# Kernel tuning notes

Hardware: AMD Instinct MI355X
Metric: run time of the kernel (lower is better)

## Reference

```python
import jax, jax.numpy as jnp
import numpy as np

D_STATE = 16
D_CONV = 4

def layernorm(x, g, b, eps=1e-5):
    m = jnp.mean(x, -1, keepdims=True)
    v = jnp.var(x, -1, keepdims=True)
    return (x - m) / jnp.sqrt(v + eps) * g + b

def conv1x1(x, w):  # x [b,h,w,cin], w [cin,cout]
    return jnp.einsum('bhwc,cd->bhwd', x, w)

def dwconv3x3(x, w):  # x [b,h,w,C], w [3,3,1,C] (HWIO, groups=C)
    return jax.lax.conv_general_dilated(x, w, (1, 1), 'SAME',
        dimension_numbers=('NHWC', 'HWIO', 'NHWC'),
        feature_group_count=x.shape[-1])

def causal_dwconv1d(x, w, b):  # x [B,L,D], w [K,1,D]; causal depthwise conv (Mamba d_conv=4)
    xp = jnp.pad(x, ((0, 0), (D_CONV - 1, 0), (0, 0)))
    y = jax.lax.conv_general_dilated(xp, w, (1,), 'VALID',
        dimension_numbers=('NWC', 'WIO', 'NWC'),
        feature_group_count=x.shape[-1])
    return y + b

def selective_scan(deltaA, deltaBx, C):
    # deltaA, deltaBx: [B,L,D,S]; C: [B,L,S] -> y: [B,L,D]
    def step(h, inp):
        dA, dBx, c = inp
        h = dA * h + dBx
        return h, jnp.einsum('bds,bs->bd', h, c)
    h0 = jnp.zeros(deltaA.shape[:1] + deltaA.shape[2:], deltaA.dtype)
    _, ys = jax.lax.scan(step, h0,
        (jnp.swapaxes(deltaA, 0, 1), jnp.swapaxes(deltaBx, 0, 1), jnp.swapaxes(C, 0, 1)))
    return jnp.swapaxes(ys, 0, 1)

def spa_ssm(x, in_w, conv_w, conv_b, xproj_w, dt_w, dt_b, Alog, D, out_w):
    # Mamba (slow path) applied to flattened spatial sequence; x: [b,h,w,c]
    b, h, w, c = x.shape
    L = h * w
    xs = x.reshape(b, L, c)
    di = Alog.shape[0]
    xz = xs @ in_w                       # [b,L,2*di]
    xi, z = xz[..., :di], xz[..., di:]
    xi = jax.nn.silu(causal_dwconv1d(xi, conv_w, conv_b))
    dbc = xi @ xproj_w                   # [b,L,dt_rank+2*S]
    dtr = dt_w.shape[0]
    dt = jax.nn.softplus(dbc[..., :dtr] @ dt_w + dt_b)   # [b,L,di]
    B = dbc[..., dtr:dtr + D_STATE]
    C = dbc[..., dtr + D_STATE:]
    A = -jnp.exp(Alog)                   # [di,S]
    deltaA = jnp.exp(dt[..., None] * A)                  # [b,L,di,S]
    deltaBx = (dt * xi)[..., None] * B[:, :, None, :]    # [b,L,di,S]
    y = selective_scan(deltaA, deltaBx, C) + D * xi
    y = y * jax.nn.silu(z)
    return (y @ out_w).reshape(b, h, w, c)

def camba_forward(x, ln1_g, ln1_b, vin_w1, vin_dw, vin_w2, vout_dw1, vout_dw2,
                  ssm_in_w, ssm_conv_w, ssm_conv_b, ssm_xproj_w, ssm_dt_w, ssm_dt_b,
                  ssm_Alog, ssm_D, ssm_out_w, ln2_g, ln2_b, ff_w1, ff_dw, ff_w2):
    x = jnp.transpose(x, (0, 2, 3, 1))   # [b,h,w,c]
    # ESSM: v_in_head = LN -> 1x1 -> dw3x3 -> GELU -> 1x1
    x0 = conv1x1(layernorm(x, ln1_g, ln1_b), vin_w1)
    x0 = jax.nn.gelu(dwconv3x3(x0, vin_dw), approximate=False)
    x0 = conv1x1(x0, vin_w2)
    y = spa_ssm(x0, ssm_in_w, ssm_conv_w, ssm_conv_b, ssm_xproj_w,
                ssm_dt_w, ssm_dt_b, ssm_Alog, ssm_D, ssm_out_w) + x0
    # v_out_head = dw3x3 -> GELU -> dw3x3, residual
    y = dwconv3x3(jax.nn.gelu(dwconv3x3(y, vout_dw1), approximate=False), vout_dw2) + y
    x = y + x                            # block residual
    # PreNorm FeedForward (mult=4): 1x1 -> LReLU -> dw3x3 -> LReLU -> 1x1
    t = layernorm(x, ln2_g, ln2_b)
    t = jax.nn.leaky_relu(conv1x1(t, ff_w1), 0.2)
    t = jax.nn.leaky_relu(dwconv3x3(t, ff_dw), 0.2)
    t = conv1x1(t, ff_w2)
    x = t + x
    return jnp.transpose(x, (0, 3, 1, 2))

def setup_inputs() -> dict:
    key = jax.random.key(0)
    ks = jax.random.split(key, 16)
    b, c, h, w = 8, 64, 64, 64
    di, ds, dtr = 128, 16, 4
    s = 0.05
    n = lambda k, shp: jax.random.normal(k, shp, jnp.float32) * s
    dt0 = jnp.exp(jax.random.uniform(ks[1], (di,)) * (np.log(0.1) - np.log(1e-3)) + np.log(1e-3))
    return dict(
        x=jax.random.normal(ks[0], (b, c, h, w), jnp.float32),
        ln1_g=jnp.ones(c), ln1_b=jnp.zeros(c),
        vin_w1=n(ks[2], (c, c)), vin_dw=n(ks[3], (3, 3, 1, c)), vin_w2=n(ks[4], (c, c)),
        vout_dw1=n(ks[5], (3, 3, 1, c)), vout_dw2=n(ks[6], (3, 3, 1, c)),
        ssm_in_w=n(ks[7], (c, 2 * di)),
        ssm_conv_w=n(ks[8], (D_CONV, 1, di)), ssm_conv_b=jnp.zeros(di),
        ssm_xproj_w=n(ks[9], (di, dtr + 2 * ds)),
        ssm_dt_w=n(ks[10], (dtr, di)), ssm_dt_b=jnp.log(jnp.expm1(dt0)),
        ssm_Alog=jnp.log(jnp.broadcast_to(jnp.arange(1., ds + 1), (di, ds))),
        ssm_D=jnp.ones(di),
        ssm_out_w=n(ks[11], (di, c)),
        ln2_g=jnp.ones(c), ln2_b=jnp.zeros(c),
        ff_w1=n(ks[12], (c, 4 * c)), ff_dw=n(ks[13], (3, 3, 1, 4 * c)), ff_w2=n(ks[14], (4 * c, c)),
    )

def reference(x, ln1_g, ln1_b, vin_w1, vin_dw, vin_w2, vout_dw1, vout_dw2,
              ssm_in_w, ssm_conv_w, ssm_conv_b, ssm_xproj_w, ssm_dt_w, ssm_dt_b,
              ssm_Alog, ssm_D, ssm_out_w, ln2_g, ln2_b, ff_w1, ff_dw, ff_w2):
    return camba_forward(x, ln1_g, ln1_b, vin_w1, vin_dw, vin_w2, vout_dw1, vout_dw2,
                         ssm_in_w, ssm_conv_w, ssm_conv_b, ssm_xproj_w, ssm_dt_w, ssm_dt_b,
                         ssm_Alog, ssm_D, ssm_out_w, ln2_g, ln2_b, ff_w1, ff_dw, ff_w2)
```

## Files before the change

kernel.cpp:

```cpp
#include <hip/hip_runtime.h>
#include <hip/hip_bf16.h>
#include <math.h>

typedef unsigned short u16;
typedef __attribute__((ext_vector_type(8))) short s8v;
typedef __attribute__((ext_vector_type(4))) float f4v;

#define B_    8
#define C_    64
#define HW_   4096
#define NPIX  32768
#define DI    128
#define NCH   256
#define CHL   16

__device__ __forceinline__ float b2f(u16 v){ return __uint_as_float(((unsigned)v)<<16); }
__device__ __forceinline__ u16 f2b(float x){
  unsigned u = __float_as_uint(x);
  u += 0x7fff + ((u >> 16) & 1);
  return (u16)(u >> 16);
}
__device__ __forceinline__ float gelu_exact(float x){ return 0.5f*x*(1.0f+erff(x*0.70710678118654752f)); }
__device__ __forceinline__ float leaky02(float x){ return x>0.f ? x : 0.2f*x; }
__device__ __forceinline__ float softplus_(float x){ return fmaxf(x,0.f)+log1pf(__expf(-fabsf(x))); }
__device__ __forceinline__ float silu_(float x){ return x / (1.0f + __expf(-x)); }
__device__ __forceinline__ void unpack16(uint4 q0, uint4 q1, float* v){
  unsigned w[8]={q0.x,q0.y,q0.z,q0.w,q1.x,q1.y,q1.z,q1.w};
  #pragma unroll
  for(int j=0;j<8;j++){
    v[2*j]   = __uint_as_float(w[j]<<16);
    v[2*j+1] = __uint_as_float(w[j]&0xffff0000u);
  }
}

__global__ void k_prep(const float* __restrict__ vin_w1, const float* __restrict__ vin_w2,
                       const float* __restrict__ ssm_in_w, const float* __restrict__ xproj,
                       const float* __restrict__ dtw, const float* __restrict__ ssm_outw,
                       const float* __restrict__ ff_w1, const float* __restrict__ ff_w2,
                       u16* __restrict__ wv1, u16* __restrict__ wv2, u16* __restrict__ wsi,
                       u16* __restrict__ wdb, u16* __restrict__ wout, u16* __restrict__ wf1,
                       u16* __restrict__ wf2t){
  int g = blockIdx.x*256 + threadIdx.x;
  if(g < 4096){
    int n=g>>6, c=g&63;
    wv1[n*64+c]=f2b(vin_w1[c*64+n]);
    wv2[n*64+c]=f2b(vin_w2[c*64+n]);
  }
  if(g < 16384){
    int n=g>>6, c=g&63;
    wsi[n*64+c]=f2b(ssm_in_w[c*256+n]);
    wf1[n*64+c]=f2b(ff_w1[c*256+n]);
    int n2=g/256, k2=g%256;
    wf2t[n2*256+k2]=f2b(ff_w2[k2*64+n2]);
  }
  if(g < 8192){
    int n=g>>7, k=g&127;
    wout[n*128+k]=f2b(ssm_outw[k*64+n]);
  }
  if(g < 20480){
    int n=g/128, k=g%128;
    float v;
    if(n < 128){
      v = 0.f;
      for(int r=0;r<4;r++) v += xproj[k*36+r]*dtw[r*128+n];
    }else{
      v = xproj[k*36+4+(n-128)];
    }
    wdb[n*128+k]=f2b(v);
  }
}

__global__ __launch_bounds__(256) void k_trans_ln_mm(const float* __restrict__ x,
                     const float* __restrict__ g, const float* __restrict__ bta,
                     const u16* __restrict__ wT,
                     u16* __restrict__ xT, u16* __restrict__ outp){
  const int LDA = 72, NS = 4;
  __shared__ float tile[64][65];
  __shared__ __align__(16) u16 sA[64*LDA];
  __shared__ __align__(16) u16 sW[64*LDA];
  int tid = threadIdx.x;
  int blk = blockIdx.x;
  int b = blk >> 6;
  int hwb = (blk & 63) << 6;
  int lane = tid & 63, row = tid >> 6;
  const float* src = x + (size_t)b*C_*HW_;
  #pragma unroll
  for(int k=0;k<16;k++){
    int c = row + 4*k;
    tile[c][lane] = src[c*HW_ + hwb + lane];
  }
  for(int idx=tid; idx<64*8; idx+=256){
    int n = idx>>3, c8 = (idx&7)*8;
    *(uint4*)(sW + n*LDA + c8) = *(const uint4*)(wT + n*64 + c8);
  }
  __syncthreads();
  u16* dstT = xT + (size_t)b*HW_*C_;
  #pragma unroll
  for(int k=0;k<16;k++){
    int hwl = row + 4*k;
    dstT[(hwb+hwl)*C_ + lane] = f2b(tile[lane][hwl]);
  }
  float gg = g[lane], bb = bta[lane];
  #pragma unroll
  for(int i=0;i<16;i++){
    int hwl = row*16 + i;
    float v = tile[lane][hwl];
    float s = v, sq = v*v;
    #pragma unroll
    for(int o=32;o>0;o>>=1){ s += __shfl_xor(s,o); sq += __shfl_xor(sq,o); }
    float m = s*(1.f/64.f);
    float var = sq*(1.f/64.f) - m*m;
    float r = rsqrtf(var + 1e-5f);
    sA[hwl*LDA + lane] = f2b((v-m)*r*gg + bb);
  }
  __syncthreads();
  int ln = tid & 63, wv = tid >> 6;
  int mrow = ln & 15, quad = ln >> 4;
  f4v acc[NS];
  #pragma unroll
  for(int i=0;i<NS;i++) acc[i] = (f4v){0.f,0.f,0.f,0.f};
  const u16* aBase = sA + (wv*16 + mrow)*LDA + quad*8;
  const u16* wBase = sW + mrow*LDA + quad*8;
  #pragma unroll
  for(int kk=0; kk<64; kk+=32){
    s8v af = *(const s8v*)(aBase + kk);
    #pragma unroll
    for(int ns=0; ns<NS; ns++){
      s8v bf = *(const s8v*)(wBase + ns*16*LDA + kk);
      acc[ns] = __builtin_amdgcn_mfma_f32_16x16x32_bf16(af, bf, acc[ns], 0, 0, 0);
    }
  }
  int p0 = blk*64;
  int pr = p0 + wv*16 + quad*4;
  #pragma unroll
  for(int ns=0; ns<NS; ns++){
    int n = ns*16 + mrow;
    #pragma unroll
    for(int r=0;r<4;r++)
      outp[(size_t)(pr+r)*64 + n] = f2b(acc[ns][r]);
  }
}

__global__ __launch_bounds__(256) void k_dw3mm(const u16* __restrict__ in,
                     const float* __restrict__ dwgt, const u16* __restrict__ wT,
                     u16* __restrict__ x0){
  const int LDT = 72;
  __shared__ __align__(16) u16 sIn[10*10*64];
  __shared__ __align__(16) u16 sT[64*LDT];
  __shared__ __align__(16) u16 sW[64*LDT];
  int tid = threadIdx.x;
  int blk = blockIdx.x;
  int b = blk >> 6;
  int t6 = blk & 63;
  int h0 = (t6 >> 3) * 8, w0 = (t6 & 7) * 8;
  for(int idx=tid; idx<64*8; idx+=256){
    int n = idx>>3, c8 = (idx&7)*8;
    *(uint4*)(sW + n*LDT + c8) = *(const uint4*)(wT + n*64 + c8);
  }
  for(int q=tid; q<10*10*16; q+=256){
    int pp = q >> 4, c4 = q & 15;
    int hh = pp / 10, ww = pp % 10;
    int gh = h0-1+hh, gw = w0-1+ww;
    ushort4 v = make_ushort4(0,0,0,0);
    if((unsigned)gh < 64u && (unsigned)gw < 64u)
      v = *(const ushort4*)(in + (size_t)((b*64+gh)*64+gw)*64 + c4*4);
    *(ushort4*)(sIn + pp*64 + c4*4) = v;
  }
  __syncthreads();
  int c4 = tid & 15;
  #pragma unroll
  for(int pass=0; pass<4; pass++){
    int opix = pass*16 + (tid>>4);
    int oh = opix >> 3, ow = opix & 7;
    float a0=0.f,a1=0.f,a2=0.f,a3=0.f;
    #pragma unroll
    for(int kh=0;kh<3;kh++){
      #pragma unroll
      for(int kw=0;kw<3;kw++){
        ushort4 v = *(const ushort4*)(sIn + ((oh+kh)*10 + (ow+kw))*64 + c4*4);
        float4 wv = *(const float4*)(dwgt + (kh*3+kw)*64 + c4*4);
        a0 += b2f(v.x)*wv.x; a1 += b2f(v.y)*wv.y;
        a2 += b2f(v.z)*wv.z; a3 += b2f(v.w)*wv.w;
      }
    }
    ushort4 o; o.x=f2b(gelu_exact(a0)); o.y=f2b(gelu_exact(a1));
    o.z=f2b(gelu_exact(a2)); o.w=f2b(gelu_exact(a3));
    *(ushort4*)(sT + opix*LDT + c4*4) = o;
  }
  __syncthreads();
  int ln = tid & 63, wv = tid >> 6;
  int mrow = ln & 15, quad = ln >> 4;
  f4v acc[4];
  #pragma unroll
  for(int i=0;i<4;i++) acc[i] = (f4v){0.f,0.f,0.f,0.f};
  const u16* aBase = sT + (wv*16 + mrow)*LDT + quad*8;
  const u16* wBase = sW + mrow*LDT + quad*8;
  #pragma unroll
  for(int kk=0; kk<64; kk+=32){
    s8v af = *(const s8v*)(aBase + kk);
    #pragma unroll
    for(int ns=0; ns<4; ns++){
      s8v bf = *(const s8v*)(wBase + ns*16*LDT + kk);
      acc[ns] = __builtin_amdgcn_mfma_f32_16x16x32_bf16(af, bf, acc[ns], 0, 0, 0);
    }
  }
  #pragma unroll
  for(int ns=0; ns<4; ns++){
    int n = ns*16 + mrow;
    #pragma unroll
    for(int r=0;r<4;r++){
      int opix = wv*16 + quad*4 + r;
      int oh = opix >> 3, ow = opix & 7;
      size_t p = ((size_t)(b*64 + h0+oh)*64 + (w0+ow));
      x0[p*64 + n] = f2b(acc[ns][r]);
    }
  }
}

template<int CIN, int COUT, int ACT, bool OUTF32>
__global__ __launch_bounds__(256) void k_mfma(const u16* __restrict__ wT,
                     const u16* __restrict__ in, const float* __restrict__ bias,
                     const u16* __restrict__ res, void* __restrict__ outv){
  const int KCH = (CIN < 128) ? CIN : 128;
  const int LDA = KCH + 8;
  const int NS  = COUT / 16;
  __shared__ __align__(16) u16 sA[64*LDA];
  __shared__ __align__(16) u16 sW[COUT*LDA];
  int tid = threadIdx.x;
  int p0 = blockIdx.x * 64;
  int ln = tid & 63, wv = tid >> 6;
  int mrow = ln & 15, quad = ln >> 4;
  f4v acc[NS];
  #pragma unroll
  for(int i=0;i<NS;i++) acc[i] = (f4v){0.f,0.f,0.f,0.f};
  const u16* aBase = sA + (wv*16 + mrow)*LDA + quad*8;
  const u16* wBase = sW + mrow*LDA + quad*8;
  const int RW = KCH/8;
  for(int k0=0; k0<CIN; k0+=KCH){
    if(k0) __syncthreads();
    for(int idx=tid; idx<COUT*RW; idx+=256){
      int n = idx/RW, c8 = (idx%RW)*8;
      *(uint4*)(sW + n*LDA + c8) = *(const uint4*)(wT + (size_t)n*CIN + k0 + c8);
    }
    for(int g=tid; g<64*RW; g+=256){
      int row = g / RW, c8 = (g % RW)*8;
      *(uint4*)(sA + row*LDA + c8) = *(const uint4*)(in + (size_t)(p0+row)*CIN + k0 + c8);
    }
    __syncthreads();
    #pragma unroll
    for(int kk=0; kk<KCH; kk+=32){
      s8v af = *(const s8v*)(aBase + kk);
      #pragma unroll
      for(int ns=0; ns<NS; ns++){
        s8v bf = *(const s8v*)(wBase + ns*16*LDA + kk);
        acc[ns] = __builtin_amdgcn_mfma_f32_16x16x32_bf16(af, bf, acc[ns], 0, 0, 0);
      }
    }
  }
  int pr = p0 + wv*16 + quad*4;
  #pragma unroll
  for(int ns=0; ns<NS; ns++){
    int n = ns*16 + mrow;
    float bs = bias ? bias[n] : 0.f;
    #pragma unroll
    for(int r=0;r<4;r++){
      float v = acc[ns][r] + bs;
      if(ACT==1) v = leaky02(v);
      else if(ACT==2) v = softplus_(v);
      if(res) v += b2f(res[(size_t)(pr+r)*COUT + n]);
      if(OUTF32) ((float*)outv)[(size_t)(pr+r)*COUT + n] = v;
      else       ((u16*)outv)[(size_t)(pr+r)*COUT + n] = f2b(v);
    }
  }
}

__global__ __launch_bounds__(256) void k_ssm_dtbc(const u16* __restrict__ wT,
                     const u16* __restrict__ x0,
                     const float* __restrict__ cw, const float* __restrict__ cb,
                     const u16* __restrict__ wdb, const float* __restrict__ dtbias,
                     u16* __restrict__ xi, u16* __restrict__ zs,
                     u16* __restrict__ dtout, u16* __restrict__ bcout){
  const int LDA=72, NS=16, LDY=136, LDWD=136, NS2=10;
  __shared__ __align__(16) u16 S[31616];
  u16* sW   = S;
  u16* sA   = S + 18432;
  u16* ubuf = S + 23040;
  u16* xiT  = S;
  u16* wdbS = S + 8704;
  int tid = threadIdx.x;
  int p0 = blockIdx.x*64;
  int ln = tid & 63, wv = tid >> 6;
  int mrow = ln & 15, quad = ln >> 4;
  for(int idx=tid; idx<256*8; idx+=256){
    int n = idx>>3, c8 = (idx&7)*8;
    *(uint4*)(sW + n*LDA + c8) = *(const uint4*)(wT + n*64 + c8);
  }
  for(int g=tid; g<64*8; g+=256){
    int row = g >> 3, c8 = (g & 7)*8;
    *(uint4*)(sA + row*LDA + c8) = *(const uint4*)(x0 + (size_t)(p0+row)*64 + c8);
  }
  __syncthreads();
  f4v acc[NS];
  #pragma unroll
  for(int i=0;i<NS;i++) acc[i] = (f4v){0.f,0.f,0.f,0.f};
  const u16* aBase = sA + (wv*16 + mrow)*LDA + quad*8;
  const u16* wBase = sW + mrow*LDA + quad*8;
  #pragma unroll
  for(int kk=0; kk<64; kk+=32){
    s8v af = *(const s8v*)(aBase + kk);
    #pragma unroll
    for(int ns=0; ns<NS; ns++){
      s8v bf = *(const s8v*)(wBase + ns*16*LDA + kk);
      acc[ns] = __builtin_amdgcn_mfma_f32_16x16x32_bf16(af, bf, acc[ns], 0, 0, 0);
    }
  }
  bool bstart = ((p0 & 4095) == 0);
  for(int idx=tid; idx<384; idx+=256){
    int j = idx >> 7, n = idx & 127;
    float a2 = 0.f;
    if(!bstart){
      const u16* xr = x0 + (size_t)(p0-3+j)*64;
      #pragma unroll 8
      for(int c=0;c<64;c++) a2 += b2f(xr[c]) * b2f(sW[n*LDA+c]);
    }
    ubuf[j*128 + n] = f2b(a2);
  }
  int prl = wv*16 + quad*4;
  #pragma unroll
  for(int ns=0; ns<NS; ns++){
    int n = ns*16 + mrow;
    if(n < 128){
      #pragma unroll
      for(int r=0;r<4;r++) ubuf[(prl+r+3)*128 + n] = f2b(acc[ns][r]);
    }else{
      #pragma unroll
      for(int r=0;r<4;r++) zs[(size_t)(p0+prl+r)*128 + (n-128)] = f2b(silu_(acc[ns][r]));
    }
  }
  __syncthreads();
  int d4 = tid & 31;
  float4 cbv = *(const float4*)(cb + d4*4);
  for(int row = tid >> 5; row < 64; row += 8){
    float a0=cbv.x, a1=cbv.y, a2=cbv.z, a3=cbv.w;
    #pragma unroll
    for(int k=0;k<4;k++){
      ushort4 v = *(const ushort4*)(ubuf + (row+k)*128 + d4*4);
      float4 wv4 = *(const float4*)(cw + k*128 + d4*4);
      a0 += b2f(v.x)*wv4.x; a1 += b2f(v.y)*wv4.y;
      a2 += b2f(v.z)*wv4.z; a3 += b2f(v.w)*wv4.w;
    }
    ushort4 o; o.x=f2b(silu_(a0)); o.y=f2b(silu_(a1)); o.z=f2b(silu_(a2)); o.w=f2b(silu_(a3));
    *(ushort4*)(xi + (size_t)(p0+row)*128 + d4*4) = o;
    *(ushort4*)(xiT + row*LDY + d4*4) = o;
  }
  __syncthreads();
  for(int idx=tid; idx<160*16; idx+=256){
    int n = idx>>4, c8 = (idx&15)*8;
    *(uint4*)(wdbS + n*LDWD + c8) = *(const uint4*)(wdb + n*128 + c8);
  }
  __syncthreads();
  f4v acc2[NS2];
  #pragma unroll
  for(int i=0;i<NS2;i++) acc2[i] = (f4v){0.f,0.f,0.f,0.f};
  #pragma unroll
  for(int kk=0; kk<128; kk+=32){
    s8v af = *(const s8v*)(xiT + (wv*16+mrow)*LDY + kk + quad*8);
    #pragma unroll
    for(int ns=0; ns<NS2; ns++){
      s8v bf = *(const s8v*)(wdbS + (ns*16+mrow)*LDWD + kk + quad*8);
      acc2[ns] = __builtin_amdgcn_mfma_f32_16x16x32_bf16(af, bf, acc2[ns], 0, 0, 0);
    }
  }
  int pr = p0 + wv*16 + quad*4;
  #pragma unroll
  for(int ns=0; ns<NS2; ns++){
    int n = ns*16 + mrow;
    if(n < 128){
      float bs = dtbias[n];
      #pragma unroll
      for(int r=0;r<4;r++)
        dtout[(size_t)(pr+r)*128 + n] = f2b(softplus_(acc2[ns][r] + bs));
    }else{
      #pragma unroll
      for(int r=0;r<4;r++)
        bcout[(size_t)(pr+r)*32 + (n-128)] = f2b(acc2[ns][r]);
    }
  }
}

__global__ __launch_bounds__(256) void k_scan1(const u16* __restrict__ dt, const u16* __restrict__ xi,
                        const u16* __restrict__ bc, const float* __restrict__ alog,
                        u16* __restrict__ Pb, u16* __restrict__ Qb){
  int t = blockIdx.x*256 + threadIdx.x;
  int d = t & 127;
  int ch = (t >> 7) & 255;
  int b = t >> 15;
  int pbase = b*HW_ + ch*CHL;
  float A[16];
  #pragma unroll
  for(int s=0;s<16;s++) A[s] = -__expf(alog[d*16+s]);
  float dtv[16], uv[16];
  #pragma unroll
  for(int i=0;i<CHL;i++){
    dtv[i] = b2f(dt[(size_t)(pbase+i)*128 + d]);
    uv[i]  = dtv[i] * b2f(xi[(size_t)(pbase+i)*128 + d]);
  }
  float Q[16], sumdt = 0.f;
  #pragma unroll
  for(int s=0;s<16;s++) Q[s] = 0.f;
  #pragma unroll
  for(int i=0;i<CHL;i++){
    float Bv[16];
    unpack16(*(const uint4*)(bc + (size_t)(pbase+i)*32),
             *(const uint4*)(bc + (size_t)(pbase+i)*32 + 8), Bv);
    sumdt += dtv[i];
    #pragma unroll
    for(int s=0;s<16;s++){
      float a = __expf(dtv[i]*A[s]);
      Q[s] = a*Q[s] + uv[i]*Bv[s];
    }
  }
  int gidx = ch*16384 + (b*128+d)*16;
  unsigned pw[8], qw[8];
  #pragma unroll
  for(int j=0;j<8;j++){
    pw[j] = (unsigned)f2b(__expf(A[2*j]*sumdt)) | ((unsigned)f2b(__expf(A[2*j+1]*sumdt))<<16);
    qw[j] = (unsigned)f2b(Q[2*j]) | ((unsigned)f2b(Q[2*j+1])<<16);
  }
  *(uint4*)(Pb+gidx)   = make_uint4(pw[0],pw[1],pw[2],pw[3]);
  *(uint4*)(Pb+gidx+8) = make_uint4(pw[4],pw[5],pw[6],pw[7]);
  *(uint4*)(Qb+gidx)   = make_uint4(qw[0],qw[1],qw[2],qw[3]);
  *(uint4*)(Qb+gidx+8) = make_uint4(qw[4],qw[5],qw[6],qw[7]);
}

__global__ void k_scan2(const u16* __restrict__ Pb, const u16* __restrict__ Qb,
                        u16* __restrict__ Hin){
  int g2 = (blockIdx.x*64 + threadIdx.x)*2;
  float h0 = 0.f, h1 = 0.f;
  #pragma unroll 8
  for(int ch=0; ch<NCH; ch++){
    unsigned p = *(const unsigned*)(Pb + ch*16384 + g2);
    unsigned q = *(const unsigned*)(Qb + ch*16384 + g2);
    *(unsigned*)(Hin + ch*16384 + g2) = (unsigned)f2b(h0) | ((unsigned)f2b(h1)<<16);
    h0 = __uint_as_float(p<<16)*h0 + __uint_as_float(q<<16);
    h1 = __uint_as_float(p&0xffff0000u)*h1 + __uint_as_float(q&0xffff0000u);
  }
}

__global__ __launch_bounds__(128) void k_scan3_mm(const u16* __restrict__ dt, const u16* __restrict__ xi,
                        const u16* __restrict__ bc, const u16* __restrict__ zs,
                        const float* __restrict__ alog, const float* __restrict__ Dp,
                        const u16* __restrict__ Hin, const u16* __restrict__ wout,
                        const u16* __restrict__ x0, u16* __restrict__ y){
  const int LDY = 136, LDW = 136;
  int blk = blockIdx.x;
  int ch = blk & (NCH-1);
  int b = blk >> 8;
  int d = threadIdx.x, tid = threadIdx.x;
  __shared__ __align__(16) u16 sY[CHL*LDY];
  __shared__ __align__(16) u16 sWo[64*LDW];
  __shared__ __align__(16) u16 sbc[CHL*32];
  for(int idx=tid; idx<64*16; idx+=128){
    int n = idx>>4, c8 = (idx&15)*8;
    *(uint4*)(sWo + n*LDW + c8) = *(const uint4*)(wout + n*128 + c8);
  }
  int pbase = b*HW_ + ch*CHL;
  if(tid < 64) ((uint4*)sbc)[tid] = ((const uint4*)(bc + (size_t)pbase*32))[tid];
  float A[16], h[16];
  u16 hbuf[16];
  int gidx = ch*16384 + (b*128+d)*16;
  *(uint4*)hbuf     = *(const uint4*)(Hin+gidx);
  *(uint4*)(hbuf+8) = *(const uint4*)(Hin+gidx+8);
  #pragma unroll
  for(int s=0;s<16;s++){ A[s] = -__expf(alog[d*16+s]); h[s] = b2f(hbuf[s]); }
  float Dd = Dp[d];
  float dtv[16], xiv[16], zsv[16];
  #pragma unroll
  for(int i=0;i<CHL;i++){
    dtv[i] = b2f(dt[(size_t)(pbase+i)*128 + d]);
    xiv[i] = b2f(xi[(size_t)(pbase+i)*128 + d]);
    zsv[i] = b2f(zs[(size_t)(pbase+i)*128 + d]);
  }
  __syncthreads();
  #pragma unroll
  for(int i=0;i<CHL;i++){
    float Bv[16], Cv[16];
    unpack16(*(const uint4*)(sbc + i*32),      *(const uint4*)(sbc + i*32 + 8),  Bv);
    unpack16(*(const uint4*)(sbc + i*32 + 16), *(const uint4*)(sbc + i*32 + 24), Cv);
    float u = dtv[i]*xiv[i];
    float acc = Dd*xiv[i];
    #pragma unroll
    for(int s=0;s<16;s++){
      float a = __expf(dtv[i]*A[s]);
      h[s] = a*h[s] + u*Bv[s];
      acc += h[s]*Cv[s];
    }
    sY[i*LDY + d] = f2b(acc * zsv[i]);
  }
  __syncthreads();
  int ln = tid & 63, wv = tid >> 6;
  int mrow = ln & 15, quad = ln >> 4;
  f4v acc2[2];
  acc2[0] = (f4v){0.f,0.f,0.f,0.f};
  acc2[1] = (f4v){0.f,0.f,0.f,0.f};
  #pragma unroll
  for(int kk=0; kk<128; kk+=32){
    s8v af = *(const s8v*)(sY + mrow*LDY + kk + quad*8);
    #pragma unroll
    for(int ns=0; ns<2; ns++){
      int n0 = wv*32 + ns*16;
      s8v bf = *(const s8v*)(sWo + (n0+mrow)*LDW + kk + quad*8);
      acc2[ns] = __builtin_amdgcn_mfma_f32_16x16x32_bf16(af, bf, acc2[ns], 0, 0, 0);
    }
  }
  #pragma unroll
  for(int ns=0; ns<2; ns++){
    int n = wv*32 + ns*16 + mrow;
    #pragma unroll
    for(int r=0;r<4;r++){
      int px = pbase + quad*4 + r;
      y[(size_t)px*64 + n] = f2b(acc2[ns][r] + b2f(x0[(size_t)px*64 + n]));
    }
  }
}

template<int COUT, int ACT>
__global__ __launch_bounds__(256) void k_mfma_ln(const u16* __restrict__ wT,
                     const u16* __restrict__ in, const float* __restrict__ g,
                     const float* __restrict__ bta, u16* __restrict__ outp){
  const int CIN = 64, LDA = 72, NS = COUT/16;
  __shared__ __align__(16) u16 sA[64*LDA];
  __shared__ __align__(16) u16 sW[COUT*LDA];
  int tid = threadIdx.x;
  int p0 = blockIdx.x * 64;
  int ln = tid & 63, wv = tid >> 6;
  int mrow = ln & 15, quad = ln >> 4;
  for(int idx=tid; idx<COUT*8; idx+=256){
    int n = idx>>3, c8 = (idx&7)*8;
    *(uint4*)(sW + n*LDA + c8) = *(const uint4*)(wT + n*64 + c8);
  }
  float gg = g[ln], bb = bta[ln];
  #pragma unroll
  for(int i=0;i<16;i++){
    int row = wv*16 + i;
    float v = b2f(in[(size_t)(p0+row)*64 + ln]);
    float s = v, sq = v*v;
    #pragma unroll
    for(int o=32;o>0;o>>=1){ s += __shfl_xor(s,o); sq += __shfl_xor(sq,o); }
    float m = s*(1.f/64.f);
    float var = sq*(1.f/64.f) - m*m;
    float r = rsqrtf(var + 1e-5f);
    sA[row*LDA + ln] = f2b((v-m)*r*gg + bb);
  }
  __syncthreads();
  f4v acc[NS];
  #pragma unroll
  for(int i=0;i<NS;i++) acc[i] = (f4v){0.f,0.f,0.f,0.f};
  const u16* aBase = sA + (wv*16 + mrow)*LDA + quad*8;
  const u16* wBase = sW + mrow*LDA + quad*8;
  #pragma unroll
  for(int kk=0; kk<CIN; kk+=32){
    s8v af = *(const s8v*)(aBase + kk);
    #pragma unroll
    for(int ns=0; ns<NS; ns++){
      s8v bf = *(const s8v*)(wBase + ns*16*LDA + kk);
      acc[ns] = __builtin_amdgcn_mfma_f32_16x16x32_bf16(af, bf, acc[ns], 0, 0, 0);
    }
  }
  int pr = p0 + wv*16 + quad*4;
  #pragma unroll
  for(int ns=0; ns<NS; ns++){
    int n = ns*16 + mrow;
    #pragma unroll
    for(int r=0;r<4;r++){
      float v = acc[ns][r];
      if(ACT==1) v = leaky02(v);
      outp[(size_t)(pr+r)*COUT + n] = f2b(v);
    }
  }
}

__global__ __launch_bounds__(256) void k_mfma_fin(const u16* __restrict__ wT,
                     const u16* __restrict__ in, const u16* __restrict__ res,
                     float* __restrict__ outp){
  const int CIN=256, COUT=64, KCH=128, LDA=136, NS=4;
  __shared__ __align__(16) u16 sA[64*LDA];
  __shared__ __align__(16) u16 sW[COUT*LDA];
  int tid = threadIdx.x;
  int p0 = blockIdx.x * 64;
  int ln = tid & 63, wv = tid >> 6;
  int mrow = ln & 15, quad = ln >> 4;
  f4v acc[NS];
  #pragma unroll
  for(int i=0;i<NS;i++) acc[i] = (f4v){0.f,0.f,0.f,0.f};
  const u16* aBase = sA + (wv*16 + mrow)*LDA + quad*8;
  const u16* wBase = sW + mrow*LDA + quad*8;
  for(int k0=0; k0<CIN; k0+=KCH){
    if(k0) __syncthreads();
    for(int idx=tid; idx<COUT*16; idx+=256){
      int n = idx>>4, c8 = (idx&15)*8;
      *(uint4*)(sW + n*LDA + c8) = *(const uint4*)(wT + n*256 + k0 + c8);
    }
    for(int g=tid; g<64*16; g+=256){
      int row = g >> 4, c8 = (g & 15)*8;
      *(uint4*)(sA + row*LDA + c8) = *(const uint4*)(in + (size_t)(p0+row)*CIN + k0 + c8);
    }
    __syncthreads();
    #pragma unroll
    for(int kk=0; kk<KCH; kk+=32){
      s8v af = *(const s8v*)(aBase + kk);
      #pragma unroll
      for(int ns=0; ns<NS; ns++){
        s8v bf = *(const s8v*)(wBase + ns*16*LDA + kk);
        acc[ns] = __builtin_amdgcn_mfma_f32_16x16x32_bf16(af, bf, acc[ns], 0, 0, 0);
      }
    }
  }
  int pr = p0 + wv*16 + quad*4;
  int b = blockIdx.x >> 6;
  int hwr = ((blockIdx.x & 63) << 6) + wv*16 + quad*4;
  #pragma unroll
  for(int ns=0; ns<NS; ns++){
    int n = ns*16 + mrow;
    float4 v4;
    v4.x = acc[ns][0] + b2f(res[(size_t)(pr+0)*64 + n]);
    v4.y = acc[ns][1] + b2f(res[(size_t)(pr+1)*64 + n]);
    v4.z = acc[ns][2] + b2f(res[(size_t)(pr+2)*64 + n]);
    v4.w = acc[ns][3] + b2f(res[(size_t)(pr+3)*64 + n]);
    *(float4*)(outp + (size_t)b*C_*HW_ + (size_t)n*HW_ + hwr) = v4;
  }
}

template<int CN, int ACT>
__global__ void k_dw3(const u16* __restrict__ in, const float* __restrict__ wgt,
                      const u16* __restrict__ res1, const u16* __restrict__ res2,
                      u16* __restrict__ out){
  const int C4 = CN/4;
  int g = blockIdx.x*256 + threadIdx.x;
  int c4 = g % C4;
  int pix = g / C4;
  int w = pix & 63;
  int h = (pix >> 6) & 63;
  int b = pix >> 12;
  float a0=0.f, a1=0.f, a2=0.f, a3=0.f;
  #pragma unroll
  for(int kh=0;kh<3;kh++){
    int hh = h + kh - 1;
    if((unsigned)hh < 64u){
      #pragma unroll
      for(int kw=0;kw<3;kw++){
        int ww = w + kw - 1;
        if((unsigned)ww < 64u){
          ushort4 v = *(const ushort4*)(in + (size_t)((b*64+hh)*64 + ww)*CN + c4*4);
          float4 wv = *(const float4*)(wgt + (kh*3+kw)*CN + c4*4);
          a0 += b2f(v.x)*wv.x; a1 += b2f(v.y)*wv.y;
          a2 += b2f(v.z)*wv.z; a3 += b2f(v.w)*wv.w;
        }
      }
    }
  }
  if(ACT==1){ a0=leaky02(a0); a1=leaky02(a1); a2=leaky02(a2); a3=leaky02(a3); }
  else if(ACT==2){ a0=gelu_exact(a0); a1=gelu_exact(a1); a2=gelu_exact(a2); a3=gelu_exact(a3); }
  size_t ob = (size_t)pix*CN + c4*4;
  if(res1){ ushort4 r = *(const ushort4*)(res1 + ob);
            a0+=b2f(r.x); a1+=b2f(r.y); a2+=b2f(r.z); a3+=b2f(r.w); }
  if(res2){ ushort4 r = *(const ushort4*)(res2 + ob);
            a0+=b2f(r.x); a1+=b2f(r.y); a2+=b2f(r.z); a3+=b2f(r.w); }
  ushort4 o; o.x=f2b(a0); o.y=f2b(a1); o.z=f2b(a2); o.w=f2b(a3);
  *(ushort4*)(out + ob) = o;
}

extern "C" void kernel_launch(void* const* d_in, const int* in_sizes, int n_in,
                              void* d_out, int out_size, void* d_ws, size_t ws_size,
                              hipStream_t stream) {
  const float* x        = (const float*)d_in[0];
  const float* ln1_g    = (const float*)d_in[1];
  const float* ln1_b    = (const float*)d_in[2];
  const float* vin_w1   = (const float*)d_in[3];
  const float* vin_dw   = (const float*)d_in[4];
  const float* vin_w2   = (const float*)d_in[5];
  const float* vout_dw1 = (const float*)d_in[6];
  const float* vout_dw2 = (const float*)d_in[7];
  const float* ssm_in_w = (const float*)d_in[8];
  const float* ssm_cw   = (const float*)d_in[9];
  const float* ssm_cb   = (const float*)d_in[10];
  const float* ssm_xprj = (const float*)d_in[11];
  const float* ssm_dtw  = (const float*)d_in[12];
  const float* ssm_dtb  = (const float*)d_in[13];
  const float* ssm_Alog = (const float*)d_in[14];
  const float* ssm_D    = (const float*)d_in[15];
  const float* ssm_outw = (const float*)d_in[16];
  const float* ln2_g    = (const float*)d_in[17];
  const float* ln2_b    = (const float*)d_in[18];
  const float* ff_w1    = (const float*)d_in[19];
  const float* ff_dw    = (const float*)d_in[20];
  const float* ff_w2    = (const float*)d_in[21];
  float* out = (float*)d_out;

  const size_t M = 1u<<20;
  u16* U   = (u16*)d_ws;
  u16* xT  = U;
  u16* tA  = U + 2*M;
  u16* tB  = U + 4*M;
  u16* x0  = U + 6*M;
  u16* xi  = U + 8*M;
  u16* zs  = U + 12*M;
  u16* xz  = U + 16*M;
  u16* dtb = U + 24*M;
  u16* bc  = U + 28*M;
  u16* Pb  = U + 16*M;
  u16* Qb  = U + 20*M;
  u16* Hin = tA;
  u16* y   = U + 16*M;
  u16* t2  = dtb;
  u16* wv1  = U + 33*M;
  u16* wv2  = wv1 + 4096;
  u16* wsi  = wv2 + 4096;
  u16* wdb  = wsi + 16384;
  u16* wout = wdb + 20480;
  u16* wf1  = wout + 8192;
  u16* wf2t = wf1 + 16384;

  k_prep<<<80,256,0,stream>>>(vin_w1, vin_w2, ssm_in_w, ssm_xprj, ssm_dtw, ssm_outw,
                              ff_w1, ff_w2, wv1, wv2, wsi, wdb, wout, wf1, wf2t);

  k_trans_ln_mm<<<512,256,0,stream>>>(x, ln1_g, ln1_b, wv1, xT, tB);
  k_dw3mm<<<512,256,0,stream>>>(tB, vin_dw, wv2, x0);

  k_ssm_dtbc<<<512,256,0,stream>>>(wsi, x0, ssm_cw, ssm_cb, wdb, ssm_dtb,
                                   xi, zs, dtb, bc);
  k_scan1<<<1024,256,0,stream>>>(dtb, xi, bc, ssm_Alog, Pb, Qb);
  k_scan2<<<128,64,0,stream>>>(Pb, Qb, Hin);
  k_scan3_mm<<<2048,128,0,stream>>>(dtb, xi, bc, zs, ssm_Alog, ssm_D, Hin, wout, x0, y);

  k_dw3<64,2><<<2048,256,0,stream>>>(y, vout_dw1, nullptr, nullptr, tA);
  k_dw3<64,0><<<2048,256,0,stream>>>(tA, vout_dw2, y, xT, x0);

  k_mfma_ln<256,1><<<512,256,0,stream>>>(wf1, x0, ln2_g, ln2_b, xz);
  k_dw3<256,1><<<8192,256,0,stream>>>(xz, ff_dw, nullptr, nullptr, t2);
  k_mfma_fin<<<512,256,0,stream>>>(wf2t, t2, x0, out);
}
```

Measured before the change: 274.3 us.

## Parallelize chunk-carry scan across chunks and fuse two depthwise convs

The sequential cross-chunk carry scan, which used 128 blocks of 64 threads each walking all 256 chunks, becomes a two-level scan. Each block stages a 32-state slice of P/Q for all chunks in shared memory, eight thread groups compose 32-chunk segments, and a short prefix over group results then seeds each group's rewrite of the incoming states. Separately, the two back-to-back 3x3 depthwise convs (GELU, then residual add) are fused into one tiled kernel that keeps the intermediate in LDS with a halo. This removes a global round trip for the intermediate and one launch, at the cost of recomputing halo pixels.

```diff
diff --git a/kernel.cpp b/kernel.cpp
--- a/kernel.cpp
+++ b/kernel.cpp
@@ -433,17 +433,43 @@
   *(uint4*)(Qb+gidx+8) = make_uint4(qw[4],qw[5],qw[6],qw[7]);
 }
 
-__global__ void k_scan2(const u16* __restrict__ Pb, const u16* __restrict__ Qb,
+__global__ __launch_bounds__(256) void k_scan2(const u16* __restrict__ Pb, const u16* __restrict__ Qb,
                         u16* __restrict__ Hin){
-  int g2 = (blockIdx.x*64 + threadIdx.x)*2;
-  float h0 = 0.f, h1 = 0.f;
+  __shared__ __align__(16) u16 sP[256*32];
+  __shared__ __align__(16) u16 sQ[256*32];
+  __shared__ float gP[8*32];
+  __shared__ float gQ[8*32];
+  int tid = threadIdx.x;
+  int s0 = blockIdx.x * 32;
+  for(int idx = tid; idx < 256*4; idx += 256){
+    int ch = idx >> 2, j8 = (idx & 3) * 8;
+    *(uint4*)(sP + ch*32 + j8) = *(const uint4*)(Pb + (size_t)ch*16384 + s0 + j8);
+    *(uint4*)(sQ + ch*32 + j8) = *(const uint4*)(Qb + (size_t)ch*16384 + s0 + j8);
+  }
+  __syncthreads();
+  int sl = tid & 31, grp = tid >> 5;
+  int base = grp * 32;
+  float P = 1.f, Q = 0.f;
   #pragma unroll 8
-  for(int ch=0; ch<NCH; ch++){
-    unsigned p = *(const unsigned*)(Pb + ch*16384 + g2);
-    unsigned q = *(const unsigned*)(Qb + ch*16384 + g2);
-    *(unsigned*)(Hin + ch*16384 + g2) = (unsigned)f2b(h0) | ((unsigned)f2b(h1)<<16);
-    h0 = __uint_as_float(p<<16)*h0 + __uint_as_float(q<<16);
-    h1 = __uint_as_float(p&0xffff0000u)*h1 + __uint_as_float(q&0xffff0000u);
+  for(int c = 0; c < 32; c++){
+    float p = b2f(sP[(base+c)*32 + sl]);
+    float q = b2f(sQ[(base+c)*32 + sl]);
+    P = p * P;
+    Q = p * Q + q;
+  }
+  gP[grp*32 + sl] = P;
+  gQ[grp*32 + sl] = Q;
+  __syncthreads();
+  float h = 0.f;
+  #pragma unroll
+  for(int g = 0; g < 7; g++){
+    if(g < grp) h = gP[g*32 + sl] * h + gQ[g*32 + sl];
+  }
+  for(int c = 0; c < 32; c++){
+    Hin[(size_t)(base+c)*16384 + s0 + sl] = f2b(h);
+    float p = b2f(sP[(base+c)*32 + sl]);
+    float q = b2f(sQ[(base+c)*32 + sl]);
+    h = p * h + q;
   }
 }
 
@@ -628,6 +654,81 @@
     v4.z = acc[ns][2] + b2f(res[(size_t)(pr+2)*64 + n]);
     v4.w = acc[ns][3] + b2f(res[(size_t)(pr+3)*64 + n]);
     *(float4*)(outp + (size_t)b*C_*HW_ + (size_t)n*HW_ + hwr) = v4;
+  }
+}
+
+__global__ __launch_bounds__(256) void k_dw3x2(const u16* __restrict__ yin,
+                      const float* __restrict__ w1, const float* __restrict__ w2,
+                      const u16* __restrict__ xTr, u16* __restrict__ outp){
+  const int LDH = 68;
+  __shared__ __align__(16) u16 sY[144*LDH];
+  __shared__ __align__(16) u16 sT[100*LDH];
+  int tid = threadIdx.x;
+  int blk = blockIdx.x;
+  int b = blk >> 6;
+  int t6 = blk & 63;
+  int h0 = (t6 >> 3) * 8, w0 = (t6 & 7) * 8;
+  for(int q=tid; q<144*16; q+=256){
+    int pp = q >> 4, c4 = q & 15;
+    int hh = pp / 12, ww = pp - hh*12;
+    int gh = h0-2+hh, gw = w0-2+ww;
+    ushort4 v = make_ushort4(0,0,0,0);
+    if((unsigned)gh < 64u && (unsigned)gw < 64u)
+      v = *(const ushort4*)(yin + (size_t)((b*64+gh)*64+gw)*64 + c4*4);
+    *(ushort4*)(sY + pp*LDH + c4*4) = v;
+  }
+  __syncthreads();
+  int c4 = tid & 15;
+  #pragma unroll
+  for(int pass=0; pass<7; pass++){
+    int tpix = pass*16 + (tid>>4);
+    if(tpix < 100){
+      int th = tpix / 10, tw = tpix - th*10;
+      int gh = h0-1+th, gw = w0-1+tw;
+      ushort4 o = make_ushort4(0,0,0,0);
+      if((unsigned)gh < 64u && (unsigned)gw < 64u){
+        float a0=0.f,a1=0.f,a2=0.f,a3=0.f;
+        #pragma unroll
+        for(int kh=0;kh<3;kh++){
+          #pragma unroll
+          for(int kw=0;kw<3;kw++){
+            ushort4 v = *(const ushort4*)(sY + ((th+kh)*12 + (tw+kw))*LDH + c4*4);
+            float4 wv = *(const float4*)(w1 + (kh*3+kw)*64 + c4*4);
+            a0 += b2f(v.x)*wv.x; a1 += b2f(v.y)*wv.y;
+            a2 += b2f(v.z)*wv.z; a3 += b2f(v.w)*wv.w;
+          }
+        }
+        o.x=f2b(gelu_exact(a0)); o.y=f2b(gelu_exact(a1));
+        o.z=f2b(gelu_exact(a2)); o.w=f2b(gelu_exact(a3));
+      }
+      *(ushort4*)(sT + tpix*LDH + c4*4) = o;
+    }
+  }
+  __syncthreads();
+  #pragma unroll
+  for(int pass=0; pass<4; pass++){
+    int opix = pass*16 + (tid>>4);
+    int oh = opix >> 3, ow = opix & 7;
+    float a0=0.f,a1=0.f,a2=0.f,a3=0.f;
+    #pragma unroll
+    for(int kh=0;kh<3;kh++){
+      #pragma unroll
+      for(int kw=0;kw<3;kw++){
+        ushort4 v = *(const ushort4*)(sT + ((oh+kh)*10 + (ow+kw))*LDH + c4*4);
+        float4 wv = *(const float4*)(w2 + (kh*3+kw)*64 + c4*4);
+        a0 += b2f(v.x)*wv.x; a1 += b2f(v.y)*wv.y;
+        a2 += b2f(v.z)*wv.z; a3 += b2f(v.w)*wv.w;
+      }
+    }
+    size_t gp = (size_t)((b*64 + h0+oh)*64 + (w0+ow));
+    ushort4 ry = *(const ushort4*)(sY + ((oh+2)*12 + (ow+2))*LDH + c4*4);
+    ushort4 rx = *(const ushort4*)(xTr + gp*64 + c4*4);
+    a0 += b2f(ry.x); a0 += b2f(rx.x);
+    a1 += b2f(ry.y); a1 += b2f(rx.y);
+    a2 += b2f(ry.z); a2 += b2f(rx.z);
+    a3 += b2f(ry.w); a3 += b2f(rx.w);
+    ushort4 o; o.x=f2b(a0); o.y=f2b(a1); o.z=f2b(a2); o.w=f2b(a3);
+    *(ushort4*)(outp + gp*64 + c4*4) = o;
   }
 }
 
@@ -730,11 +831,10 @@
   k_ssm_dtbc<<<512,256,0,stream>>>(wsi, x0, ssm_cw, ssm_cb, wdb, ssm_dtb,
                                    xi, zs, dtb, bc);
   k_scan1<<<1024,256,0,stream>>>(dtb, xi, bc, ssm_Alog, Pb, Qb);
-  k_scan2<<<128,64,0,stream>>>(Pb, Qb, Hin);
+  k_scan2<<<512,256,0,stream>>>(Pb, Qb, Hin);
   k_scan3_mm<<<2048,128,0,stream>>>(dtb, xi, bc, zs, ssm_Alog, ssm_D, Hin, wout, x0, y);
 
-  k_dw3<64,2><<<2048,256,0,stream>>>(y, vout_dw1, nullptr, nullptr, tA);
-  k_dw3<64,0><<<2048,256,0,stream>>>(tA, vout_dw2, y, xT, x0);
+  k_dw3x2<<<512,256,0,stream>>>(y, vout_dw1, vout_dw2, xT, x0);
 
   k_mfma_ln<256,1><<<512,256,0,stream>>>(wf1, x0, ln2_g, ln2_b, xz);
   k_dw3<256,1><<<8192,256,0,stream>>>(xz, ff_dw, nullptr, nullptr, t2);
```

New measurement: 261.2 us. -4.8%, faster.
